# Performance work log

Hardware: AMD Instinct MI355X
Metric: run time of the kernel (lower is better)

## Reference

```python
import jax, jax.numpy as jnp
import numpy as np
import math

DIM = 1024
CHUNK = 64
B, S = 4, 4096

def setup_inputs() -> dict:
    key = jax.random.key(0)
    ks = jax.random.split(key, 16)
    d = DIM
    std = 1.0 / math.sqrt(d)
    def lin(k):
        k1, k2 = jax.random.split(k)
        return (jax.random.uniform(k1, (d, d), jnp.float32, -std, std),
                jax.random.uniform(k2, (d,), jnp.float32, -std, std))
    Wk, bk = lin(ks[0])
    Wv, bv = lin(ks[1])
    Wq, bq = lin(ks[2])
    Wkp, bkp = lin(ks[3])
    Wqp, bqp = lin(ks[4])
    Wo, bo = lin(ks[5])
    return {
        "x": jax.random.normal(ks[6], (B, S, d), jnp.float32),
        "Wk": Wk, "bk": bk, "Wv": Wv, "bv": bv, "Wq": Wq, "bq": bq,
        "Wkp": Wkp, "bkp": bkp, "Wqp": Wqp, "bqp": bqp,
        "phase_scale": jnp.full((d,), math.pi, jnp.float32),
        "ln_g": jnp.ones((d,), jnp.float32),
        "ln_b": jnp.zeros((d,), jnp.float32),
        "Wo": Wo, "bo": bo,
    }

def _linear(x, W, b):
    # torch nn.Linear: x @ W.T + b
    return jnp.einsum('bsd,ed->bse', x, W) + b

def _layernorm(x, g, b, eps=1e-5):
    mu = jnp.mean(x, axis=-1, keepdims=True)
    var = jnp.var(x, axis=-1, keepdims=True)
    return (x - mu) * jax.lax.rsqrt(var + eps) * g + b

def reference(x, Wk, bk, Wv, bv, Wq, bq, Wkp, bkp, Wqp, bqp,
              phase_scale, ln_g, ln_b, Wo, bo):
    batch, seq_len, dim = x.shape
    key = _linear(x, Wk, bk)
    value = _linear(x, Wv, bv)
    query = _linear(x, Wq, bq)
    key_phase = jnp.tanh(_linear(key, Wkp, bkp)) * phase_scale
    query_phase = jnp.tanh(_linear(query, Wqp, bqp)) * phase_scale
    bound_real = value * jnp.cos(key_phase)
    bound_imag = value * jnpp_sin(key_phase) if False else value * jnp.sin(key_phase)
    pad_len = (CHUNK - seq_len % CHUNK) % CHUNK
    if pad_len > 0:
        pad = ((0, 0), (0, pad_len), (0, 0))
        bound_real = jnp.pad(bound_real, pad)
        bound_imag = jnp.pad(bound_imag, pad)
        query_phase = jnp.pad(query_phase, pad)
    padded_len = bound_real.shape[1]
    nc = padded_len // CHUNK
    br = bound_real.reshape(batch, nc, CHUNK, dim)
    bi = bound_imag.reshape(batch, nc, CHUNK, dim)
    qp = query_phase.reshape(batch, nc, CHUNK, dim)
    mem_real = jnp.cumsum(br, axis=2)
    mem_imag = jnp.cumsum(bi, axis=2)
    retrieved = mem_real * jnp.cos(qp) + mem_imag * jnp.sin(qp)
    retrieved = retrieved.reshape(batch, padded_len, dim)[:, :seq_len]
    retrieved = retrieved / math.sqrt(dim)
    out = _linear(_layernorm(retrieved, ln_g, ln_b), Wo, bo)
    return x + out
```

## Files before the change

kernel.cpp:

```cpp
#include <hip/hip_runtime.h>
#include <math.h>

#define DIMD 1024
#define CHUNKLEN 64
#define NTOK 16384

#define TM 128
#define TN 128
#define BK 64

typedef __bf16 bf16x8 __attribute__((ext_vector_type(8)));
typedef float floatx4 __attribute__((ext_vector_type(4)));
typedef unsigned short ushort8v __attribute__((ext_vector_type(8)));

__device__ __forceinline__ float bf2f(unsigned short u) {
  union { unsigned int i; float f; } v; v.i = ((unsigned int)u) << 16; return v.f;
}
__device__ __forceinline__ unsigned short f2bf(float f) {
  union { float f; unsigned int i; } v; v.f = f;
  unsigned int r = v.i + 0x7FFFu + ((v.i >> 16) & 1u);
  return (unsigned short)(r >> 16);
}

__device__ __forceinline__ float tanh_fast(float v) {
  const float t = __expf(2.0f * v);
  return 1.0f - 2.0f * __builtin_amdgcn_rcpf(t + 1.0f);
}

__device__ __forceinline__ void async16(const unsigned short* g, unsigned short* l) {
  __builtin_amdgcn_global_load_lds(
      (const __attribute__((address_space(1))) unsigned int*)g,
      (__attribute__((address_space(3))) unsigned int*)l, 16, 0, 0);
}

__global__ __launch_bounds__(256) void cvt_all_kernel(
    const float* __restrict__ x,
    const float* __restrict__ w0, const float* __restrict__ w1,
    const float* __restrict__ w2, const float* __restrict__ w3,
    unsigned short* __restrict__ dx,
    unsigned short* __restrict__ d0, unsigned short* __restrict__ d1,
    unsigned short* __restrict__ d2, unsigned short* __restrict__ d3)
{
  const int b = blockIdx.x;
  const float* src; unsigned short* dst; long i;
  if (b < 16384) {
    src = x; dst = dx; i = (long)b * 256 + threadIdx.x;
  } else {
    const int r = b - 16384;
    const int s = r >> 10;
    src = s == 0 ? w0 : s == 1 ? w1 : s == 2 ? w2 : w3;
    dst = s == 0 ? d0 : s == 1 ? d1 : s == 2 ? d2 : d3;
    i = (long)(r & 1023) * 256 + threadIdx.x;
  }
  const float4 v = ((const float4*)src)[i];
  ushort4 o;
  o.x = f2bf(v.x); o.y = f2bf(v.y); o.z = f2bf(v.z); o.w = f2bf(v.w);
  ((ushort4*)dst)[i] = o;
}

__global__ __launch_bounds__(256) void transpose_cvt_kernel(
    const float* __restrict__ s0, const float* __restrict__ s1,
    unsigned short* __restrict__ q0, unsigned short* __restrict__ q1)
{
  __shared__ unsigned short tile[64][66];
  const float* src = blockIdx.z ? s1 : s0;
  unsigned short* dst = blockIdx.z ? q1 : q0;
  const int e0 = blockIdx.y * 64;
  const int k0 = blockIdx.x * 64;
  const int t  = threadIdx.x;
  const int tr = t >> 4;
  const int tc = t & 15;
#pragma unroll
  for (int p = 0; p < 4; ++p) {
    const int el = p * 16 + tr;
    const float4 v = *(const float4*)&src[(long)(e0 + el) * DIMD + k0 + tc * 4];
    tile[el][tc * 4 + 0] = f2bf(v.x);
    tile[el][tc * 4 + 1] = f2bf(v.y);
    tile[el][tc * 4 + 2] = f2bf(v.z);
    tile[el][tc * 4 + 3] = f2bf(v.w);
  }
  __syncthreads();
#pragma unroll
  for (int p = 0; p < 4; ++p) {
    const int kl = p * 16 + tr;
    ushort4 o;
    o.x = tile[tc * 4 + 0][kl];
    o.y = tile[tc * 4 + 1][kl];
    o.z = tile[tc * 4 + 2][kl];
    o.w = tile[tc * 4 + 3][kl];
    *(ushort4*)&dst[(long)(k0 + kl) * DIMD + e0 + tc * 4] = o;
  }
}

__global__ __launch_bounds__(256) void bias_comb_kernel(
    const float* __restrict__ Wkp, const float* __restrict__ bk,
    const float* __restrict__ bkp,
    const float* __restrict__ Wqp, const float* __restrict__ bq,
    const float* __restrict__ bqp,
    float* __restrict__ bkq, float* __restrict__ bqq)
{
  const int b = blockIdx.x;
  const int which = b >> 8;
  const int lane = threadIdx.x & 63;
  const int wid  = threadIdx.x >> 6;
  const int n = (b & 255) * 4 + wid;
  const float* W    = which ? Wqp : Wkp;
  const float* bvec = which ? bq  : bk;
  const float* badd = which ? bqp : bkp;
  float*       outp = which ? bqq : bkq;
  float s = 0.f;
#pragma unroll
  for (int i = 0; i < 16; ++i)
    s += W[(long)n * DIMD + lane + i * 64] * bvec[lane + i * 64];
#pragma unroll
  for (int o = 32; o > 0; o >>= 1) s += __shfl_xor(s, o, 64);
  if (lane == 0) outp[n] = s + badd[n];
}

template <int MODE>
__global__ __launch_bounds__(256) void gemm_bt_kernel(
    const unsigned short* __restrict__ A0, const unsigned short* __restrict__ A1,
    const unsigned short* __restrict__ W0, const unsigned short* __restrict__ W1,
    const unsigned short* __restrict__ W2,
    const float* __restrict__ b0, const float* __restrict__ b1,
    const float* __restrict__ b2,
    const float* __restrict__ aux,
    unsigned short* __restrict__ O0, unsigned short* __restrict__ O1,
    unsigned short* __restrict__ O2,
    float* __restrict__ Of, const float* __restrict__ resid)
{
  __shared__ unsigned short lsA[TM * BK];
  __shared__ unsigned short lsB[TN * BK];

  const int tid  = threadIdx.x;
  const int lane = tid & 63;
  const int wid  = tid >> 6;
  const long bm  = (long)blockIdx.y * TM;
  const long bng = (long)blockIdx.x * TN;

  const unsigned short* A = A0;
  const unsigned short* W = W0;
  const float* bias = b0;
  unsigned short* Ob = O0;
  long bn = bng;
  int seg = 0;
  if (MODE == 0) {
    seg = (int)(bng >> 10);
    bn = bng & 1023;
    W    = seg == 0 ? W0 : (seg == 1 ? W1 : W2);
    bias = seg == 0 ? b0 : (seg == 1 ? b1 : b2);
    Ob   = seg == 0 ? O0 : (seg == 1 ? O1 : O2);
  } else if (MODE == 1) {
    if (blockIdx.z) { A = A1; W = W1; Ob = O1; }
  }

  const int wm = (wid & 1) * 64;
  const int wn = (wid >> 1) * 64;

  floatx4 acc[4][4];
#pragma unroll
  for (int i = 0; i < 4; ++i)
#pragma unroll
    for (int j = 0; j < 4; ++j)
      acc[i][j] = (floatx4)(0.0f);

  const int srow  = lane >> 3;
  const int pcol  = (lane & 7) * 8;
  const int lcolL = (((lane & 7) ^ (srow & 7)) * 8);
  const int frm   = lane & 15;
  const int cfrk  = lane >> 4;

  for (int kk = 0; kk < DIMD; kk += BK) {
    __syncthreads();
#pragma unroll
    for (int j = 0; j < 4; ++j) {
      const int inst = wid * 4 + j;
      const int r = inst * 8 + srow;
      async16(A + (bm + r) * (long)DIMD + kk + lcolL, &lsA[r * BK + pcol]);
      async16(W + (bn + r) * (long)DIMD + kk + lcolL, &lsB[r * BK + pcol]);
    }
    __syncthreads();
#pragma unroll
    for (int ks = 0; ks < BK; ks += 32) {
      const int cb  = (ks >> 3) + cfrk;
      const int swz = ((cb ^ (frm & 7)) << 3);
      bf16x8 af[4], bfr[4];
#pragma unroll
      for (int i = 0; i < 4; ++i)
        af[i]  = *(const bf16x8*)&lsA[(wm + i * 16 + frm) * BK + swz];
#pragma unroll
      for (int i = 0; i < 4; ++i)
        bfr[i] = *(const bf16x8*)&lsB[(wn + i * 16 + frm) * BK + swz];
#pragma unroll
      for (int i = 0; i < 4; ++i)
#pragma unroll
        for (int j = 0; j < 4; ++j)
          acc[i][j] = __builtin_amdgcn_mfma_f32_16x16x32_bf16(af[i], bfr[j], acc[i][j], 0, 0, 0);
    }
  }

  const int cn = lane & 15;
  const int rq = (lane >> 4) * 4;
#pragma unroll
  for (int j = 0; j < 4; ++j) {
    const long col = bn + wn + j * 16 + cn;
    const float bv = (MODE == 1) ? 0.0f : bias[col];
    const float pv = (MODE == 0) ? aux[col] : 0.0f;
#pragma unroll
    for (int i = 0; i < 4; ++i) {
#pragma unroll
      for (int r = 0; r < 4; ++r) {
        const long row = bm + wm + i * 16 + rq + r;
        const float v = acc[i][j][r] + bv;
        if (MODE == 0) {
          Ob[row * (long)DIMD + col] = (seg == 0) ? f2bf(v)
                                                  : f2bf(tanh_fast(v) * pv);
        } else if (MODE == 1) {
          Ob[row * (long)DIMD + col] = f2bf(v);
        } else {
          Of[row * (long)DIMD + col] = v + resid[row * (long)DIMD + col];
        }
      }
    }
  }
}

#define TILE16 16384
#define HALF16 8192

template <int MODE>
__global__ __launch_bounds__(512, 2) void gemm256_kernel(
    const unsigned short* __restrict__ A,
    const unsigned short* __restrict__ W0, const unsigned short* __restrict__ W1,
    const unsigned short* __restrict__ W2,
    const float* __restrict__ b0, const float* __restrict__ b1,
    const float* __restrict__ b2,
    const float* __restrict__ aux,
    unsigned short* __restrict__ O0, unsigned short* __restrict__ O1,
    unsigned short* __restrict__ O2,
    float* __restrict__ Of, const float* __restrict__ resid)
{
  __shared__ unsigned short lds[4 * TILE16];

  const int tid  = threadIdx.x;
  const int lane = tid & 63;
  const int wid  = tid >> 6;

  constexpr int NBX = (MODE == 0) ? 12 : 4;
  constexpr int NWG = NBX * 64;
  const int orig = blockIdx.x + blockIdx.y * gridDim.x;
  const int swzb = (orig & 7) * (NWG >> 3) + (orig >> 3);
  const int nb = swzb % NBX;
  const int mb = swzb / NBX;

  const long bm = (long)mb * 256;
  long bn;
  int seg = 0;
  const unsigned short* W = W0;
  const float* bias = b0;
  unsigned short* Ob = O0;
  if (MODE == 0) {
    seg = nb >> 2;
    bn  = (long)(nb & 3) * 256;
    W    = seg == 0 ? W0 : (seg == 1 ? W1 : W2);
    bias = seg == 0 ? b0 : (seg == 1 ? b1 : b2);
    Ob   = seg == 0 ? O0 : (seg == 1 ? O1 : O2);
  } else {
    bn = (long)nb * 256;
  }

  const int wm = (wid >> 2) * 128;
  const int wn = (wid & 3) * 64;

  const int q0  = wid * 2;
  const int sr0 = q0 * 16 + (lane >> 2);
  const int sg  = (((lane & 3) ^ ((sr0 >> 1) & 3)) * 8);
  const int sd0 = q0 * 512 + lane * 8;
  const long arow = (bm + sr0) * (long)DIMD;
  const long brow = (bn + sr0) * (long)DIMD;

  const int frm   = lane & 15;
  const int cfrk  = lane >> 4;
  const int slot8 = (cfrk ^ ((frm >> 1) & 3)) * 8;
  const int rbase = frm * 32 + slot8;

  floatx4 acc[8][4];
#pragma unroll
  for (int i = 0; i < 8; ++i)
#pragma unroll
    for (int j = 0; j < 4; ++j) acc[i][j] = (floatx4)(0.0f);

  bf16x8 bfr[4];

#define SA256(buf, kk, h) do { \
    const unsigned short* _s = A + arow + (kk) + (h) * 32 + sg; \
    unsigned short* _d = &lds[(buf) * TILE16 + (h) * HALF16 + sd0]; \
    async16(_s, _d); \
    async16(_s + 16 * DIMD, _d + 512); \
  } while (0)
#define SB256(buf, kk, h) do { \
    const unsigned short* _s = W + brow + (kk) + (h) * 32 + sg; \
    unsigned short* _d = &lds[2 * TILE16 + (buf) * TILE16 + (h) * HALF16 + sd0]; \
    async16(_s, _d); \
    async16(_s + 16 * DIMD, _d + 512); \
  } while (0)
#define WAITBAR() do { \
    asm volatile("s_waitcnt vmcnt(6)" ::: "memory"); \
    __builtin_amdgcn_s_barrier(); \
    asm volatile("" ::: "memory"); \
    __builtin_amdgcn_sched_barrier(0); \
  } while (0)
#define BARC() do { \
    asm volatile("" ::: "memory"); \
    __builtin_amdgcn_s_barrier(); \
    asm volatile("" ::: "memory"); \
  } while (0)
#define PHASE256(buf, h, ih, LOADB) do { \
    bf16x8 af[4]; \
    const int _ab = (buf) * TILE16 + (h) * HALF16 + (wm + (ih) * 64) * 32 + rbase; \
    _Pragma("unroll") \
    for (int i = 0; i < 4; ++i) af[i] = *(const bf16x8*)&lds[_ab + i * 512]; \
    if (LOADB) { \
      const int _bb = 2 * TILE16 + (buf) * TILE16 + (h) * HALF16 + wn * 32 + rbase; \
      _Pragma("unroll") \
      for (int j = 0; j < 4; ++j) bfr[j] = *(const bf16x8*)&lds[_bb + j * 512]; \
    } \
    __builtin_amdgcn_s_setprio(1); \
    _Pragma("unroll") \
    for (int i = 0; i < 4; ++i) \
      _Pragma("unroll") \
      for (int j = 0; j < 4; ++j) \
        acc[(ih) * 4 + i][j] = __builtin_amdgcn_mfma_f32_16x16x32_bf16( \
            af[i], bfr[j], acc[(ih) * 4 + i][j], 0, 0, 0); \
    __builtin_amdgcn_s_setprio(0); \
  } while (0)

  SA256(0, 0, 0); SB256(0, 0, 0); SA256(0, 0, 1); SB256(0, 0, 1);

#pragma unroll 1
  for (int t = 0; t < 16; t += 2) {
    const int k1 = (t + 1) * 64;
    const int k2 = (t + 2 < 16) ? (t + 2) * 64 : 0;
    SA256(1, k1, 0); WAITBAR(); PHASE256(0, 0, 0, true);  BARC();
    SB256(1, k1, 0); BARC();    PHASE256(0, 0, 1, false); BARC();
    SA256(1, k1, 1); WAITBAR(); PHASE256(0, 1, 0, true);  BARC();
    SB256(1, k1, 1); BARC();    PHASE256(0, 1, 1, false); BARC();
    SA256(0, k2, 0); WAITBAR(); PHASE256(1, 0, 0, true);  BARC();
    SB256(0, k2, 0); BARC();    PHASE256(1, 0, 1, false); BARC();
    SA256(0, k2, 1); WAITBAR(); PHASE256(1, 1, 0, true);  BARC();
    SB256(0, k2, 1); BARC();    PHASE256(1, 1, 1, false); BARC();
  }
  asm volatile("s_waitcnt vmcnt(0)" ::: "memory");

#undef SA256
#undef SB256
#undef WAITBAR
#undef BARC
#undef PHASE256

  const int cn = lane & 15;
  const int rq = (lane >> 4) * 4;
#pragma unroll
  for (int j = 0; j < 4; ++j) {
    const long col = bn + wn + j * 16 + cn;
    const float bv = bias[col];
    const float pv = (MODE == 0) ? aux[col] : 0.0f;
#pragma unroll
    for (int ii = 0; ii < 8; ++ii) {
#pragma unroll
      for (int r = 0; r < 4; ++r) {
        const long row = bm + wm + ii * 16 + rq + r;
        const float v = acc[ii][j][r] + bv;
        if (MODE == 0) {
          Ob[row * (long)DIMD + col] = (seg == 0) ? f2bf(v)
                                                  : f2bf(tanh_fast(v) * pv);
        } else {
          Of[row * (long)DIMD + col] = v + resid[row * (long)DIMD + col];
        }
      }
    }
  }
}

__global__ __launch_bounds__(512) void scan_ln_kernel(
    const unsigned short* __restrict__ V,  const unsigned short* __restrict__ KP,
    const unsigned short* __restrict__ QP,
    const float* __restrict__ lng, const float* __restrict__ lnb,
    unsigned short* __restrict__ out)
{
  __shared__ unsigned short ret_s[32][DIMD];

  const int tid  = threadIdx.x;
  const int lane = tid & 63;
  const int wid  = tid >> 6;
  const long rowBase = (long)blockIdx.x * CHUNKLEN;
  const int d0 = tid * 2;

  const int c0 = lane * 8;
  const int c1 = 512 + lane * 8;
  float g0[8], be0[8], g1[8], be1[8];
#pragma unroll
  for (int j = 0; j < 8; ++j) {
    g0[j] = lng[c0 + j]; be0[j] = lnb[c0 + j];
    g1[j] = lng[c1 + j]; be1[j] = lnb[c1 + j];
  }

  float mr[2] = {0.f, 0.f};
  float mi[2] = {0.f, 0.f};

  for (int h = 0; h < 2; ++h) {
    for (int tl = 0; tl < 32; ++tl) {
      const int t = h * 32 + tl;
      const long off = (rowBase + t) * DIMD + d0;
      const ushort2 v2 = *(const ushort2*)(V + off);
      const ushort2 k2 = *(const ushort2*)(KP + off);
      const ushort2 q2 = *(const ushort2*)(QP + off);
      const unsigned short va[2] = {v2.x, v2.y};
      const unsigned short ka[2] = {k2.x, k2.y};
      const unsigned short qa[2] = {q2.x, q2.y};
      unsigned short rv[2];
#pragma unroll
      for (int j = 0; j < 2; ++j) {
        const float v  = bf2f(va[j]);
        const float kp = bf2f(ka[j]);
        const float qp = bf2f(qa[j]);
        float skp, ckp, sqp, cqp;
        __sincosf(kp, &skp, &ckp);
        __sincosf(qp, &sqp, &cqp);
        mr[j] += v * ckp;
        mi[j] += v * skp;
        rv[j] = f2bf((mr[j] * cqp + mi[j] * sqp) * 0.03125f);
      }
      ushort2 o2; o2.x = rv[0]; o2.y = rv[1];
      *(ushort2*)&ret_s[tl][d0] = o2;
    }
    __syncthreads();

#pragma unroll 1
    for (int rr = 0; rr < 4; ++rr) {
      const int tl = wid * 4 + rr;
      const ushort8v a0 = *(const ushort8v*)&ret_s[tl][c0];
      const ushort8v a1 = *(const ushort8v*)&ret_s[tl][c1];
      float f0[8], f1[8];
      float s = 0.f, s2 = 0.f;
#pragma unroll
      for (int j = 0; j < 8; ++j) {
        f0[j] = bf2f(a0[j]); f1[j] = bf2f(a1[j]);
        s += f0[j] + f1[j];
        s2 += f0[j] * f0[j] + f1[j] * f1[j];
      }
#pragma unroll
      for (int o = 32; o > 0; o >>= 1) {
        s  += __shfl_xor(s,  o, 64);
        s2 += __shfl_xor(s2, o, 64);
      }
      const float mu  = s * (1.0f / DIMD);
      const float var = s2 * (1.0f / DIMD) - mu * mu;
      const float inv = rsqrtf(var + 1e-5f);
      ushort8v o0, o1;
#pragma unroll
      for (int j = 0; j < 8; ++j) {
        o0[j] = f2bf((f0[j] - mu) * inv * g0[j] + be0[j]);
        o1[j] = f2bf((f1[j] - mu) * inv * g1[j] + be1[j]);
      }
      const long gro = (rowBase + h * 32 + tl) * DIMD;
      *(ushort8v*)(out + gro + c0) = o0;
      *(ushort8v*)(out + gro + c1) = o1;
    }
    __syncthreads();
  }
}

extern "C" void kernel_launch(void* const* d_in, const int* in_sizes, int n_in,
                              void* d_out, int out_size, void* d_ws, size_t ws_size,
                              hipStream_t stream)
{
  const float* x   = (const float*)d_in[0];
  const float* Wk  = (const float*)d_in[1];
  const float* bk  = (const float*)d_in[2];
  const float* Wv  = (const float*)d_in[3];
  const float* bv  = (const float*)d_in[4];
  const float* Wq  = (const float*)d_in[5];
  const float* bq  = (const float*)d_in[6];
  const float* Wkp = (const float*)d_in[7];
  const float* bkp = (const float*)d_in[8];
  const float* Wqp = (const float*)d_in[9];
  const float* bqp = (const float*)d_in[10];
  const float* ph  = (const float*)d_in[11];
  const float* lng = (const float*)d_in[12];
  const float* lnb = (const float*)d_in[13];
  const float* Wo  = (const float*)d_in[14];
  const float* bo  = (const float*)d_in[15];
  float* out = (float*)d_out;

  const long NB = (long)NTOK * DIMD;
  const long DD = (long)DIMD * DIMD;
  const size_t required = (size_t)(4 * NB + 8 * DD) * sizeof(unsigned short)
                        + 2048 * sizeof(float);
  if (ws_size < required) return;

  unsigned short* S0   = (unsigned short*)d_ws;
  unsigned short* SV   = S0   + NB;
  unsigned short* SKP  = SV   + NB;
  unsigned short* SQP  = SKP  + NB;
  unsigned short* Wvb  = SQP  + NB;
  unsigned short* Wob  = Wvb  + DD;
  unsigned short* Wkpb = Wob  + DD;
  unsigned short* Wqpb = Wkpb + DD;
  unsigned short* WkT  = Wqpb + DD;
  unsigned short* WqT  = WkT  + DD;
  unsigned short* Wkqb = WqT  + DD;
  unsigned short* Wqqb = Wkqb + DD;
  float* bkq = (float*)(Wqqb + DD);
  float* bqq = bkq + DIMD;

  dim3 blk(256);

  cvt_all_kernel<<<dim3(16384 + 4 * 1024), blk, 0, stream>>>(
      x, Wv, Wo, Wkp, Wqp, S0, Wvb, Wob, Wkpb, Wqpb);
  transpose_cvt_kernel<<<dim3(16, 16, 2), blk, 0, stream>>>(Wk, Wq, WkT, WqT);
  bias_comb_kernel<<<dim3(512), blk, 0, stream>>>(Wkp, bk, bkp, Wqp, bq, bqp, bkq, bqq);
  gemm_bt_kernel<1><<<dim3(DIMD / TN, DIMD / TM, 2), blk, 0, stream>>>(
      Wkpb, Wqpb, WkT, WqT, nullptr, nullptr, nullptr, nullptr, nullptr,
      Wkqb, Wqqb, nullptr, nullptr, nullptr);
  gemm256_kernel<0><<<dim3(12, NTOK / 256), dim3(512), 0, stream>>>(
      S0, Wvb, Wkqb, Wqqb, bv, bkq, bqq, ph, SV, SKP, SQP, nullptr, nullptr);
  scan_ln_kernel<<<dim3(NTOK / CHUNKLEN), dim3(512), 0, stream>>>(
      SV, SKP, SQP, lng, lnb, S0);
  gemm256_kernel<2><<<dim3(4, NTOK / 256), dim3(512), 0, stream>>>(
      S0, Wob, nullptr, nullptr, bo, nullptr, nullptr, nullptr,
      nullptr, nullptr, nullptr, out, x);
}
```

Baseline: 410.6 us.

## Restructure GEMM main loop to issue LDS reads before async loads and barriers

Reorders each GEMM phase so LDS fragment reads are issued first, then the next async global-to-LDS copy, then a barrier and an lgkmcnt wait before the MFMAs. The vmcnt wait moves to after the B-tile copy with a looser count, and a prologue wait plus barrier is added. The intent is to hide LDS read latency behind the global copy issue and barrier, and to reduce stalls on outstanding memory operations. The epilogue is also reordered to hoist bias and aux loads and iterate rows in the outer loop for better store locality. Changing the wait counts risks races on the double-buffered LDS tiles if the ordering is off.

```diff
diff --git a/kernel.cpp b/kernel.cpp
--- a/kernel.cpp
+++ b/kernel.cpp
@@ -304,78 +304,97 @@
     async16(_s, _d); \
     async16(_s + 16 * DIMD, _d + 512); \
   } while (0)
-#define WAITBAR() do { \
-    asm volatile("s_waitcnt vmcnt(6)" ::: "memory"); \
-    __builtin_amdgcn_s_barrier(); \
-    asm volatile("" ::: "memory"); \
-    __builtin_amdgcn_sched_barrier(0); \
-  } while (0)
-#define BARC() do { \
+#define RDA256(buf, h, ih, af) do { \
+    const int _ab = (buf) * TILE16 + (h) * HALF16 + (wm + (ih) * 64) * 32 + rbase; \
+    _Pragma("unroll") \
+    for (int _i = 0; _i < 4; ++_i) (af)[_i] = *(const bf16x8*)&lds[_ab + _i * 512]; \
+  } while (0)
+#define RDB256(buf, h) do { \
+    const int _bb = 2 * TILE16 + (buf) * TILE16 + (h) * HALF16 + wn * 32 + rbase; \
+    _Pragma("unroll") \
+    for (int _j = 0; _j < 4; ++_j) bfr[_j] = *(const bf16x8*)&lds[_bb + _j * 512]; \
+  } while (0)
+#define VMW4() asm volatile("s_waitcnt vmcnt(4)" ::: "memory")
+#define BAR256() do { \
     asm volatile("" ::: "memory"); \
     __builtin_amdgcn_s_barrier(); \
     asm volatile("" ::: "memory"); \
   } while (0)
-#define PHASE256(buf, h, ih, LOADB) do { \
-    bf16x8 af[4]; \
-    const int _ab = (buf) * TILE16 + (h) * HALF16 + (wm + (ih) * 64) * 32 + rbase; \
-    _Pragma("unroll") \
-    for (int i = 0; i < 4; ++i) af[i] = *(const bf16x8*)&lds[_ab + i * 512]; \
-    if (LOADB) { \
-      const int _bb = 2 * TILE16 + (buf) * TILE16 + (h) * HALF16 + wn * 32 + rbase; \
-      _Pragma("unroll") \
-      for (int j = 0; j < 4; ++j) bfr[j] = *(const bf16x8*)&lds[_bb + j * 512]; \
-    } \
+#define LG0() do { \
+    asm volatile("s_waitcnt lgkmcnt(0)" ::: "memory"); \
+    __builtin_amdgcn_sched_barrier(0); \
+  } while (0)
+#define MFMA16(ih, af) do { \
     __builtin_amdgcn_s_setprio(1); \
     _Pragma("unroll") \
-    for (int i = 0; i < 4; ++i) \
+    for (int _i = 0; _i < 4; ++_i) \
       _Pragma("unroll") \
-      for (int j = 0; j < 4; ++j) \
-        acc[(ih) * 4 + i][j] = __builtin_amdgcn_mfma_f32_16x16x32_bf16( \
-            af[i], bfr[j], acc[(ih) * 4 + i][j], 0, 0, 0); \
+      for (int _j = 0; _j < 4; ++_j) \
+        acc[(ih) * 4 + _i][_j] = __builtin_amdgcn_mfma_f32_16x16x32_bf16( \
+            (af)[_i], bfr[_j], acc[(ih) * 4 + _i][_j], 0, 0, 0); \
     __builtin_amdgcn_s_setprio(0); \
   } while (0)
 
   SA256(0, 0, 0); SB256(0, 0, 0); SA256(0, 0, 1); SB256(0, 0, 1);
+  VMW4();
+  BAR256();
 
 #pragma unroll 1
   for (int t = 0; t < 16; t += 2) {
     const int k1 = (t + 1) * 64;
     const int k2 = (t + 2 < 16) ? (t + 2) * 64 : 0;
-    SA256(1, k1, 0); WAITBAR(); PHASE256(0, 0, 0, true);  BARC();
-    SB256(1, k1, 0); BARC();    PHASE256(0, 0, 1, false); BARC();
-    SA256(1, k1, 1); WAITBAR(); PHASE256(0, 1, 0, true);  BARC();
-    SB256(1, k1, 1); BARC();    PHASE256(0, 1, 1, false); BARC();
-    SA256(0, k2, 0); WAITBAR(); PHASE256(1, 0, 0, true);  BARC();
-    SB256(0, k2, 0); BARC();    PHASE256(1, 0, 1, false); BARC();
-    SA256(0, k2, 1); WAITBAR(); PHASE256(1, 1, 0, true);  BARC();
-    SB256(0, k2, 1); BARC();    PHASE256(1, 1, 1, false); BARC();
+    {
+      { bf16x8 af[4]; RDA256(0, 0, 0, af); RDB256(0, 0); SA256(1, k1, 0);
+        BAR256(); LG0(); MFMA16(0, af); BAR256(); }
+      { bf16x8 af[4]; RDA256(0, 0, 1, af); SB256(1, k1, 0); VMW4();
+        BAR256(); LG0(); MFMA16(1, af); BAR256(); }
+      { bf16x8 af[4]; RDA256(0, 1, 0, af); RDB256(0, 1); SA256(1, k1, 1);
+        BAR256(); LG0(); MFMA16(0, af); BAR256(); }
+      { bf16x8 af[4]; RDA256(0, 1, 1, af); SB256(1, k1, 1); VMW4();
+        BAR256(); LG0(); MFMA16(1, af); BAR256(); }
+      { bf16x8 af[4]; RDA256(1, 0, 0, af); RDB256(1, 0); SA256(0, k2, 0);
+        BAR256(); LG0(); MFMA16(0, af); BAR256(); }
+      { bf16x8 af[4]; RDA256(1, 0, 1, af); SB256(0, k2, 0); VMW4();
+        BAR256(); LG0(); MFMA16(1, af); BAR256(); }
+      { bf16x8 af[4]; RDA256(1, 1, 0, af); RDB256(1, 1); SA256(0, k2, 1);
+        BAR256(); LG0(); MFMA16(0, af); BAR256(); }
+      { bf16x8 af[4]; RDA256(1, 1, 1, af); SB256(0, k2, 1); VMW4();
+        BAR256(); LG0(); MFMA16(1, af); BAR256(); }
+    }
   }
   asm volatile("s_waitcnt vmcnt(0)" ::: "memory");
 
 #undef SA256
 #undef SB256
-#undef WAITBAR
-#undef BARC
-#undef PHASE256
+#undef RDA256
+#undef RDB256
+#undef VMW4
+#undef BAR256
+#undef LG0
+#undef MFMA16
 
   const int cn = lane & 15;
   const int rq = (lane >> 4) * 4;
+  long colj[4]; float bvj[4], pvj[4];
 #pragma unroll
   for (int j = 0; j < 4; ++j) {
-    const long col = bn + wn + j * 16 + cn;
-    const float bv = bias[col];
-    const float pv = (MODE == 0) ? aux[col] : 0.0f;
-#pragma unroll
-    for (int ii = 0; ii < 8; ++ii) {
-#pragma unroll
-      for (int r = 0; r < 4; ++r) {
-        const long row = bm + wm + ii * 16 + rq + r;
-        const float v = acc[ii][j][r] + bv;
+    colj[j] = bn + wn + j * 16 + cn;
+    bvj[j]  = bias[colj[j]];
+    pvj[j]  = (MODE == 0) ? aux[colj[j]] : 0.0f;
+  }
+#pragma unroll
+  for (int ii = 0; ii < 8; ++ii) {
+#pragma unroll
+    for (int r = 0; r < 4; ++r) {
+      const long rowo = (bm + wm + ii * 16 + rq + r) * (long)DIMD;
+#pragma unroll
+      for (int j = 0; j < 4; ++j) {
+        const float v = acc[ii][j][r] + bvj[j];
         if (MODE == 0) {
-          Ob[row * (long)DIMD + col] = (seg == 0) ? f2bf(v)
-                                                  : f2bf(tanh_fast(v) * pv);
+          Ob[rowo + colj[j]] = (seg == 0) ? f2bf(v)
+                                          : f2bf(tanh_fast(v) * pvj[j]);
         } else {
-          Of[row * (long)DIMD + col] = v + resid[row * (long)DIMD + col];
+          Of[rowo + colj[j]] = v + resid[rowo + colj[j]];
         }
       }
     }
```

Result: faster. 360.6 us (-12.2%).
